# Performance work log

Hardware: AMD Instinct MI355X
Metric: run time of the kernel (lower is better)

## Reference

```python
import jax, jax.numpy as jnp
import numpy as np

B, H, W, C = 4, 128, 128, 180
HEADS, WS = 6, 16
HID = 720            # int(dim * mlp_ratio)
CONV_SCALE = 0.01
N = WS * WS          # tokens per window
CM = C // 2          # CAB mid channels (is_light_sr -> compress_ratio=2)
CS = C // 30         # channel-attention squeeze channels


def conv2d(x, w, b=None, padding=0, dilation=1, groups=1):
    out = jax.lax.conv_general_dilated(
        x, w, (1, 1), [(padding, padding), (padding, padding)],
        rhs_dilation=(dilation, dilation),
        dimension_numbers=('NCHW', 'OIHW', 'NCHW'),
        feature_group_count=groups)
    if b is not None:
        out = out + b[None, :, None, None]
    return out


def layernorm(x, g, b, eps=1e-5):
    mu = jnp.mean(x, -1, keepdims=True)
    var = jnp.var(x, -1, keepdims=True)
    return (x - mu) * jax.lax.rsqrt(var + eps) * g + b


def make_rpi(ws):
    coords = np.stack(np.meshgrid(np.arange(ws), np.arange(ws), indexing='ij'))
    cf = coords.reshape(2, -1)
    rel = (cf[:, :, None] - cf[:, None, :]).transpose(1, 2, 0).astype(np.int64)
    rel[:, :, 0] += ws - 1
    rel[:, :, 1] += ws - 1
    rel[:, :, 0] *= 2 * ws - 1
    return rel.sum(-1)  # [n, n]


def _forward(rpi_sa, x, norm1_g, norm1_b, rpb_table, qkv_w, qkv_b, proj_w, proj_b,
             cab_w0, cab_b0, cab_w1, cab_b1, cab_w2, cab_b2, cab_w3, cab_b3,
             ca_w1, ca_b1, ca_w2, ca_b2, norm2_g, norm2_b,
             fc1_w, fc1_b, dw_w, dw_b, pw_w, pw_b, sa_w, fc2_w, fc2_b):
    b = x.shape[0]
    shortcut = x
    xn = layernorm(x, norm1_g, norm1_b)
    x_img = xn.reshape(b, H, W, C)

    # --- window partition (shift_size=0 -> no roll, no mask) ---
    xw = x_img.reshape(b, H // WS, WS, W // WS, WS, C)
    xw = xw.transpose(0, 1, 3, 2, 4, 5).reshape(-1, N, C)  # [b*nW, n, C]

    # --- window attention with relative position bias ---
    hd = C // HEADS
    qkv = (xw @ qkv_w.T + qkv_b).reshape(-1, N, 3, HEADS, hd)
    qkv = qkv.transpose(2, 0, 3, 1, 4)  # [3, b*nW, heads, n, hd]
    q, k, v = qkv[0], qkv[1], qkv[2]
    attn = jnp.einsum('whnd,whmd->whnm', q * (hd ** -0.5), k)
    bias = rpb_table[rpi_sa.reshape(-1)].reshape(N, N, HEADS).transpose(2, 0, 1)
    attn = jax.nn.softmax(attn + bias[None], axis=-1)
    out = jnp.einsum('whnm,whmd->whnd', attn, v)
    out = out.transpose(0, 2, 1, 3).reshape(-1, N, C)
    out = out @ proj_w.T + proj_b

    # --- window reverse ---
    attn_x = out.reshape(b, H // WS, W // WS, WS, WS, C)
    attn_x = attn_x.transpose(0, 1, 3, 2, 4, 5).reshape(b, H * W, C)

    # --- CAB conv branch on norm1 output (light-SR variant) ---
    x2d = x_img.transpose(0, 3, 1, 2)  # NCHW
    y = conv2d(x2d, cab_w0, cab_b0)                                  # 1x1 C->C/2
    y = conv2d(y, cab_w1, cab_b1, padding=1, groups=CM)              # dw 3x3
    y = jax.nn.gelu(y, approximate=False)
    y = conv2d(y, cab_w2, cab_b2)                                    # 1x1 C/2->C
    y = conv2d(y, cab_w3, cab_b3, padding=2, dilation=2, groups=C)   # dw 3x3 dil2
    a = jnp.mean(y, (2, 3), keepdims=True)                           # GAP
    a = jax.nn.relu(conv2d(a, ca_w1, ca_b1))
    a = jax.nn.sigmoid(conv2d(a, ca_w2, ca_b2))
    conv_x = (y * a).transpose(0, 2, 3, 1).reshape(b, H * W, C)

    x = shortcut + attn_x + conv_x * CONV_SCALE

    # --- DSConvAttnFFN ---
    xn2 = layernorm(x, norm2_g, norm2_b)
    hdn = jax.nn.gelu(xn2 @ fc1_w.T + fc1_b, approximate=False)
    h2d = hdn.reshape(b, H, W, HID).transpose(0, 3, 1, 2)
    h2d = jax.nn.relu(conv2d(h2d, dw_w, dw_b, padding=1, groups=HID))
    h2d = jax.nn.relu(conv2d(h2d, pw_w, pw_b))
    mp = jnp.max(h2d, 1, keepdims=True)
    ap = jnp.mean(h2d, 1, keepdims=True)
    sa = jax.nn.sigmoid(conv2d(jnp.concatenate([mp, ap], 1), sa_w, padding=3))
    h2d = h2d * sa
    hdn = h2d.transpose(0, 2, 3, 1).reshape(b, H * W, HID)
    return x + (hdn @ fc2_w.T + fc2_b)


def setup_inputs():
    key = jax.random.key(0)
    ks = iter(jax.random.split(key, 48))
    def w(*shape):
        return jax.random.normal(next(ks), shape, jnp.float32) * 0.02
    return dict(
        x=jax.random.normal(next(ks), (B, H * W, C), jnp.float32),
        x_size_h=H, x_size_w=W,
        rpi_sa=jnp.asarray(make_rpi(WS)),
        norm1_g=jnp.ones((C,), jnp.float32), norm1_b=jnp.zeros((C,), jnp.float32),
        rpb_table=w((2 * WS - 1) ** 2, HEADS),
        qkv_w=w(3 * C, C), qkv_b=jnp.zeros((3 * C,), jnp.float32),
        proj_w=w(C, C), proj_b=jnp.zeros((C,), jnp.float32),
        cab_w0=w(CM, C, 1, 1), cab_b0=jnp.zeros((CM,), jnp.float32),
        cab_w1=w(CM, 1, 3, 3), cab_b1=jnp.zeros((CM,), jnp.float32),
        cab_w2=w(C, CM, 1, 1), cab_b2=jnp.zeros((C,), jnp.float32),
        cab_w3=w(C, 1, 3, 3), cab_b3=jnp.zeros((C,), jnp.float32),
        ca_w1=w(CS, C, 1, 1), ca_b1=jnp.zeros((CS,), jnp.float32),
        ca_w2=w(C, CS, 1, 1), ca_b2=jnp.zeros((C,), jnp.float32),
        norm2_g=jnp.ones((C,), jnp.float32), norm2_b=jnp.zeros((C,), jnp.float32),
        fc1_w=w(HID, C), fc1_b=jnp.zeros((HID,), jnp.float32),
        dw_w=w(HID, 1, 3, 3), dw_b=jnp.zeros((HID,), jnp.float32),
        pw_w=w(HID, HID, 1, 1), pw_b=jnp.zeros((HID,), jnp.float32),
        sa_w=w(1, 2, 7, 7),
        fc2_w=w(C, HID), fc2_b=jnp.zeros((C,), jnp.float32),
    )


def reference(x, x_size_h, x_size_w, rpi_sa, norm1_g, norm1_b, rpb_table,
              qkv_w, qkv_b, proj_w, proj_b,
              cab_w0, cab_b0, cab_w1, cab_b1, cab_w2, cab_b2, cab_w3, cab_b3,
              ca_w1, ca_b1, ca_w2, ca_b2, norm2_g, norm2_b,
              fc1_w, fc1_b, dw_w, dw_b, pw_w, pw_b, sa_w, fc2_w, fc2_b):
    del x_size_h, x_size_w  # fixed to H, W
    return _forward(rpi_sa, x, norm1_g, norm1_b, rpb_table, qkv_w, qkv_b,
                    proj_w, proj_b, cab_w0, cab_b0, cab_w1, cab_b1, cab_w2,
                    cab_b2, cab_w3, cab_b3, ca_w1, ca_b1, ca_w2, ca_b2,
                    norm2_g, norm2_b, fc1_w, fc1_b, dw_w, dw_b, pw_w, pw_b,
                    sa_w, fc2_w, fc2_b)
```

## Files before the change

### kernel.cpp

```cpp
#include <hip/hip_runtime.h>
#include <math.h>

#define HH 128
#define WW 128
#define CC 180
#define BB 4
#define IMG (HH*WW)
#define NTOK (BB*IMG)
#define HALFTOK (2*IMG)
#define NHEADS 6
#define HD 30
#define WSZ 16
#define NTOKW (WSZ*WSZ)
#define HID 720
#define QKVSTR 672

typedef __attribute__((ext_vector_type(8))) short short8v;
typedef __attribute__((ext_vector_type(4))) short short4v;
typedef __attribute__((ext_vector_type(4))) float f32x4;
typedef unsigned short ushortw;

__device__ __forceinline__ float warp_sum(float v) {
    #pragma unroll
    for (int o = 32; o > 0; o >>= 1) v += __shfl_xor(v, o);
    return v;
}
__device__ __forceinline__ float warp_max(float v) {
    #pragma unroll
    for (int o = 32; o > 0; o >>= 1) v = fmaxf(v, __shfl_xor(v, o));
    return v;
}
__device__ __forceinline__ float gelu_exact(float v) {
    return 0.5f * v * (1.f + erff(v * 0.70710678118654752f));
}
__device__ __forceinline__ ushortw f2bf(float f) {
    union { float f; unsigned int u; } c; c.f = f;
    unsigned int r = (c.u + 0x7FFFu + ((c.u >> 16) & 1u)) >> 16;
    return (ushortw)r;
}
__device__ __forceinline__ float bf2f(ushortw u) {
    union { unsigned int u; float f; } c; c.u = ((unsigned int)u) << 16; return c.f;
}

__global__ __launch_bounds__(256) void prep_kernel(
    const float* __restrict__ qkv_w, const float* __restrict__ proj_w,
    const float* __restrict__ cab_w0, const float* __restrict__ cab_b0,
    const float* __restrict__ cab_w2,
    const float* __restrict__ fc1_w, const float* __restrict__ pw_w,
    const float* __restrict__ fc2_w,
    const float* __restrict__ cab_w1, const float* __restrict__ cab_b1,
    const float* __restrict__ cab_w3, const float* __restrict__ cab_b3,
    const float* __restrict__ dw_w, const float* __restrict__ dw_b,
    const float* __restrict__ qkv_b, const int* __restrict__ rpi,
    const float* __restrict__ rpb,
    ushortw* __restrict__ wqkvc, ushortw* __restrict__ wproj,
    ushortw* __restrict__ wcab2,
    ushortw* __restrict__ wfc1, ushortw* __restrict__ wpw, ushortw* __restrict__ wfc2,
    float* __restrict__ dwt1, float* __restrict__ db1,
    float* __restrict__ dwt2, float* __restrict__ db2,
    float* __restrict__ dwt3, float* __restrict__ db3,
    float* __restrict__ qb672, float* __restrict__ biasN)
{
    int idx = blockIdx.x * 256 + threadIdx.x;
    if (idx < 129024) {
        int r = idx / 192, k = idx - r * 192;
        float v = 0.f;
        if (r < 576) {
            int sub = r / 192, rem = r - sub * 192;
            int hh = rem >> 5, dd = rem & 31;
            if (dd < 30 && k < 180) v = qkv_w[(sub * 180 + hh * 30 + dd) * 180 + k];
        } else if (r < 666) {
            if (k < 180) v = cab_w0[(r - 576) * 180 + k];
        }
        wqkvc[idx] = f2bf(v);
    } else if (idx < 178176) {
        int l = idx - 129024; int r = l / 192, k = l - r * 192;
        wproj[l] = f2bf((r < 180 && k < 180) ? proj_w[r * 180 + k] : 0.f);
    } else if (idx < 210944) {
        int l = idx - 178176; int r = l / 128, k = l - r * 128;
        wcab2[l] = f2bf((r < 180 && k < 90) ? cab_w2[r * 90 + k] : 0.f);
    } else if (idx < 358400) {
        int l = idx - 210944; int r = l / 192, k = l - r * 192;
        wfc1[l] = f2bf((r < 720 && k < 180) ? fc1_w[r * 180 + k] : 0.f);
    } else if (idx < 948224) {
        int l = idx - 358400; int r = l / 768, k = l - r * 768;
        wpw[l] = f2bf((r < 720 && k < 720) ? pw_w[r * 720 + k] : 0.f);
    } else if (idx < 1144832) {
        int l = idx - 948224; int r = l / 768, k = l - r * 768;
        wfc2[l] = f2bf((r < 180 && k < 720) ? fc2_w[r * 720 + k] : 0.f);
    } else if (idx < 1145984) {
        int l = idx - 1144832; int c = l / 9, k = l - c * 9;
        dwt1[k * 128 + c] = (c < 90) ? cab_w1[c * 9 + k] : 0.f;
        if (k == 0) db1[c] = (c < 90) ? cab_b1[c] : 0.f;
    } else if (idx < 1147712) {
        int l = idx - 1145984; int c = l / 9, k = l - c * 9;
        dwt2[k * 192 + c] = (c < 180) ? cab_w3[c * 9 + k] : 0.f;
        if (k == 0) db2[c] = (c < 180) ? cab_b3[c] : 0.f;
    } else if (idx < 1154624) {
        int l = idx - 1147712; int c = l / 9, k = l - c * 9;
        dwt3[k * 768 + c] = (c < 720) ? dw_w[c * 9 + k] : 0.f;
        if (k == 0) db3[c] = (c < 720) ? dw_b[c] : 0.f;
    } else if (idx < 1155296) {
        int l = idx - 1154624;
        float v = 0.f;
        if (l < 576) {
            int sub = l / 192, rem = l - sub * 192;
            int hh = rem >> 5, dd = rem & 31;
            if (dd < 30) v = qkv_b[sub * 180 + hh * 30 + dd];
        } else if (l < 666) {
            v = cab_b0[l - 576];
        }
        qb672[l] = v;
    } else if (idx < 1220832) {
        int l = idx - 1155296;
        int r = rpi[l];
        #pragma unroll
        for (int h = 0; h < NHEADS; h++)
            biasN[((size_t)h << 16) + l] = rpb[r * NHEADS + h];
    }
}

__global__ __launch_bounds__(256) void ln_kernel(
    const float* __restrict__ x, const float* __restrict__ g,
    const float* __restrict__ b, ushortw* __restrict__ out)
{
    int wid = threadIdx.x >> 6, lane = threadIdx.x & 63;
    int t = blockIdx.x * 4 + wid;
    size_t off = (size_t)t * CC;
    size_t off2 = (size_t)t * 192;
    bool has2 = lane < (CC - 128);
    float v0 = x[off + lane];
    float v1 = x[off + lane + 64];
    float v2 = has2 ? x[off + lane + 128] : 0.f;
    float s = warp_sum(v0 + v1 + v2);
    float mu = s * (1.f / CC);
    float d0 = v0 - mu, d1 = v1 - mu, d2 = has2 ? v2 - mu : 0.f;
    float var = warp_sum(d0*d0 + d1*d1 + d2*d2) * (1.f / CC);
    float rs = rsqrtf(var + 1e-5f);
    out[off2 + lane]      = f2bf(d0 * rs * g[lane]      + b[lane]);
    out[off2 + lane + 64] = f2bf(d1 * rs * g[lane + 64] + b[lane + 64]);
    out[off2 + lane + 128] = has2 ? f2bf(d2 * rs * g[lane + 128] + b[lane + 128]) : (ushortw)0;
}

__global__ __launch_bounds__(256) void mgemm_kernel(
    const ushortw* __restrict__ A, const ushortw* __restrict__ Wt,
    const float* __restrict__ bias, void* __restrict__ Cout,
    int M, int N, int Kp, int ldc, int outbf, int zfill, int act, int residbf, int nN,
    const float* __restrict__ rowscale, const void* __restrict__ residv)
{
    __shared__ ushortw sA[2][128 * 32];
    __shared__ ushortw sB[2][128 * 32];
    int tid = threadIdx.x, lane = tid & 63, wid = tid >> 6;
    int total = (int)gridDim.x;
    int orig = blockIdx.x;
    int q = total >> 3, r = total & 7;
    int xcd = orig & 7, slot = orig >> 3;
    int wgid = (xcd < r ? xcd * (q + 1) : r * (q + 1) + (xcd - r) * q) + slot;
    int mp = wgid / nN, np = wgid - mp * nN;
    int m0 = mp << 7, n0 = np << 7;
    int wm = (wid >> 1) << 6, wn = (wid & 1) << 6;
    int lrow = lane & 15, kgrp = lane >> 4;

    f32x4 acc[4][4];
    #pragma unroll
    for (int i = 0; i < 4; i++)
        #pragma unroll
        for (int j = 0; j < 4; j++)
            #pragma unroll
            for (int rr = 0; rr < 4; rr++) acc[i][j][rr] = 0.f;

    int nk = Kp >> 5;
    #pragma unroll
    for (int qq = 0; qq < 2; qq++) {
        int seg = (wid << 1) + qq;
        int row = (seg << 4) + (lane >> 2);
        int cg = (lane & 3) ^ (row & 3) ^ ((row >> 2) & 3);
        const ushortw* ga = A + (size_t)(m0 + row) * Kp + (cg << 3);
        __builtin_amdgcn_global_load_lds(
            (const __attribute__((address_space(1))) void*)ga,
            (__attribute__((address_space(3))) void*)&sA[0][seg << 9], 16, 0, 0);
        const ushortw* gb = Wt + (size_t)(n0 + row) * Kp + (cg << 3);
        __builtin_amdgcn_global_load_lds(
            (const __attribute__((address_space(1))) void*)gb,
            (__attribute__((address_space(3))) void*)&sB[0][seg << 9], 16, 0, 0);
    }
    __syncthreads();

    int cur = 0;
    for (int t = 0; t < nk; t++) {
        if (t + 1 < nk) {
            int kk2 = (t + 1) << 5;
            #pragma unroll
            for (int qq = 0; qq < 2; qq++) {
                int seg = (wid << 1) + qq;
                int row = (seg << 4) + (lane >> 2);
                int cg = (lane & 3) ^ (row & 3) ^ ((row >> 2) & 3);
                const ushortw* ga = A + (size_t)(m0 + row) * Kp + kk2 + (cg << 3);
                __builtin_amdgcn_global_load_lds(
                    (const __attribute__((address_space(1))) void*)ga,
                    (__attribute__((address_space(3))) void*)&sA[cur ^ 1][seg << 9], 16, 0, 0);
                const ushortw* gb = Wt + (size_t)(n0 + row) * Kp + kk2 + (cg << 3);
                __builtin_amdgcn_global_load_lds(
                    (const __attribute__((address_space(1))) void*)gb,
                    (__attribute__((address_space(3))) void*)&sB[cur ^ 1][seg << 9], 16, 0, 0);
            }
        }
        short8v a[4], b[4];
        #pragma unroll
        for (int i = 0; i < 4; i++) {
            int rr = wm + (i << 4) + lrow;
            int slot2 = kgrp ^ (rr & 3) ^ ((rr >> 2) & 3);
            a[i] = *reinterpret_cast<const short8v*>(&sA[cur][(rr << 5) + (slot2 << 3)]);
        }
        #pragma unroll
        for (int j = 0; j < 4; j++) {
            int rr = wn + (j << 4) + lrow;
            int slot2 = kgrp ^ (rr & 3) ^ ((rr >> 2) & 3);
            b[j] = *reinterpret_cast<const short8v*>(&sB[cur][(rr << 5) + (slot2 << 3)]);
        }
        #pragma unroll
        for (int i = 0; i < 4; i++)
            #pragma unroll
            for (int j = 0; j < 4; j++)
                acc[i][j] = __builtin_amdgcn_mfma_f32_16x16x32_bf16(a[i], b[j], acc[i][j], 0, 0, 0);
        __syncthreads();
        cur ^= 1;
    }
    #pragma unroll
    for (int i = 0; i < 4; i++) {
        int rowb = m0 + wm + (i << 4) + (kgrp << 2);
        #pragma unroll
        for (int j = 0; j < 4; j++) {
            int col = n0 + wn + (j << 4) + lrow;
            if (col < N) {
                float bi = bias[col];
                #pragma unroll
                for (int rr = 0; rr < 4; rr++) {
                    int row = rowb + rr;
                    float v = acc[i][j][rr];
                    if (rowscale) v *= rowscale[row];
                    v += bi;
                    if (act == 1) v = gelu_exact(v);
                    else if (act == 2) v = fmaxf(v, 0.f);
                    if (residv) {
                        v += residbf ? bf2f(((const ushortw*)residv)[(size_t)row * N + col])
                                     : ((const float*)residv)[(size_t)row * N + col];
                    }
                    if (outbf) ((ushortw*)Cout)[(size_t)row * ldc + col] = f2bf(v);
                    else       ((float*)Cout)[(size_t)row * ldc + col] = v;
                }
            } else if (zfill && col < ldc) {
                #pragma unroll
                for (int rr = 0; rr < 4; rr++) {
                    int row = rowb + rr;
                    if (outbf) ((ushortw*)Cout)[(size_t)row * ldc + col] = 0;
                    else       ((float*)Cout)[(size_t)row * ldc + col] = 0.f;
                }
            }
        }
    }
}

__global__ __launch_bounds__(256, 3) void attn_mfma_kernel(
    const ushortw* __restrict__ qkvP, const float* __restrict__ biasN,
    ushortw* __restrict__ out)
{
    __shared__ ushortw Vc[32 * 33 * 8];
    __shared__ ushortw Kc[256 * 32];
    __shared__ ushortw Pl[4][2048];
    const float SCALE = 0.18257418583505536f;
    int blk = blockIdx.x;
    int img = blk / 384;
    int rem = blk - img * 384;
    int win = rem / NHEADS;
    int h = rem - win * NHEADS;
    int base = img * IMG + (win >> 3) * WSZ * WW + (win & 7) * WSZ;
    int tid = threadIdx.x;
    int lane = tid & 63, w = tid >> 6;
    int a15 = lane & 15, kg = lane >> 4;

    {
        int j = tid;
        int g = base + (j >> 4) * WW + (j & 15);
        const ushortw* vp = qkvP + (size_t)g * QKVSTR + 384 + h * 32;
        short8v c0 = *reinterpret_cast<const short8v*>(vp);
        short8v c1 = *reinterpret_cast<const short8v*>(vp + 8);
        short8v c2 = *reinterpret_cast<const short8v*>(vp + 16);
        short8v c3 = *reinterpret_cast<const short8v*>(vp + 24);
        int bo = (j >> 3) * 264 + (j & 7);
        #pragma unroll
        for (int e = 0; e < 8; e++)  Vc[bo + (e) * 8]      = (ushortw)c0[e];
        #pragma unroll
        for (int e = 0; e < 8; e++)  Vc[bo + (8 + e) * 8]  = (ushortw)c1[e];
        #pragma unroll
        for (int e = 0; e < 8; e++)  Vc[bo + (16 + e) * 8] = (ushortw)c2[e];
        #pragma unroll
        for (int e = 0; e < 8; e++)  Vc[bo + (24 + e) * 8] = (ushortw)c3[e];
        const ushortw* kp = qkvP + (size_t)g * QKVSTR + 192 + h * 32;
        short8v k0 = *reinterpret_cast<const short8v*>(kp);
        short8v k1 = *reinterpret_cast<const short8v*>(kp + 8);
        short8v k2 = *reinterpret_cast<const short8v*>(kp + 16);
        short8v k3 = *reinterpret_cast<const short8v*>(kp + 24);
        short8v* krow = reinterpret_cast<short8v*>(&Kc[j * 32]);
        int jsw = j & 3;
        krow[0 ^ jsw] = k0; krow[1 ^ jsw] = k1; krow[2 ^ jsw] = k2; krow[3 ^ jsw] = k3;
    }
    __syncthreads();

    ushortw* Pw = &Pl[w][0];
    int xsw = (a15 & 7) << 2;
    f32x4 zf = {0.f, 0.f, 0.f, 0.f};
    #pragma unroll 1
    for (int si = 0; si < 4; si++) {
        int strip = (w << 2) + si;
        short8v qf = *reinterpret_cast<const short8v*>(
            qkvP + (size_t)(base + strip * WW + a15) * QKVSTR + h * 32 + (kg << 3));
        float psum = 0.f;
        f32x4 o0 = zf, o1 = zf;
        const float* brow = biasN + ((size_t)h << 16) + (size_t)((strip << 4) + a15) * 256;
        #pragma unroll 1
        for (int half = 0; half < 2; half++) {
            f32x4 s[8];
            __builtin_amdgcn_s_setprio(1);
            #pragma unroll
            for (int j8 = 0; j8 < 8; j8++) {
                int jt = (half << 3) + j8;
                int row = (jt << 4) + a15;
                short8v ka = reinterpret_cast<const short8v*>(&Kc[row * 32])[kg ^ (row & 3)];
                s[j8] = __builtin_amdgcn_mfma_f32_16x16x32_bf16(ka, qf, zf, 0, 0, 0);
            }
            __builtin_amdgcn_s_setprio(0);
            #pragma unroll
            for (int j8 = 0; j8 < 8; j8++) {
                int jt = (half << 3) + j8;
                float4 b4 = *reinterpret_cast<const float4*>(brow + (jt << 4) + (kg << 2));
                float p0 = __expf(fmaf(s[j8][0], SCALE, b4.x));
                float p1 = __expf(fmaf(s[j8][1], SCALE, b4.y));
                float p2 = __expf(fmaf(s[j8][2], SCALE, b4.z));
                float p3 = __expf(fmaf(s[j8][3], SCALE, b4.w));
                psum += (p0 + p1) + (p2 + p3);
                unsigned int u0, u1;
                asm("v_cvt_pk_bf16_f32 %0, %1, %2" : "=v"(u0) : "v"(p0), "v"(p1));
                asm("v_cvt_pk_bf16_f32 %0, %1, %2" : "=v"(u1) : "v"(p2), "v"(p3));
                int dw0 = ((j8 << 3) + (kg << 1)) ^ xsw;
                unsigned long long pk64 = (unsigned long long)u0 | ((unsigned long long)u1 << 32);
                *reinterpret_cast<unsigned long long*>(&Pw[(a15 << 7) + (dw0 << 1)]) = pk64;
            }
            __builtin_amdgcn_sched_barrier(0);
            __builtin_amdgcn_s_setprio(1);
            #pragma unroll
            for (int ks4 = 0; ks4 < 4; ks4++) {
                int dwr = ((ks4 << 4) + (kg << 2)) ^ xsw;
                short8v pa = *reinterpret_cast<const short8v*>(&Pw[(a15 << 7) + (dwr << 1)]);
                int kc = (((half << 2) + ks4) << 2) + kg;
                short8v v0 = *reinterpret_cast<const short8v*>(&Vc[(kc * 33 + a15) * 8]);
                short8v v1 = *reinterpret_cast<const short8v*>(&Vc[(kc * 33 + 16 + a15) * 8]);
                o0 = __builtin_amdgcn_mfma_f32_16x16x32_bf16(pa, v0, o0, 0, 0, 0);
                o1 = __builtin_amdgcn_mfma_f32_16x16x32_bf16(pa, v1, o1, 0, 0, 0);
            }
            __builtin_amdgcn_s_setprio(0);
            __builtin_amdgcn_sched_barrier(0);
        }
        psum += __shfl_xor(psum, 16);
        psum += __shfl_xor(psum, 32);
        #pragma unroll
        for (int r = 0; r < 4; r++) {
            float pt = __shfl(psum, (kg << 2) + r);
            float inv = 1.f / pt;
            int g = base + strip * WW + (kg << 2) + r;
            ushortw* orow = out + (size_t)g * 192 + h * HD;
            orow[a15] = f2bf(o0[r] * inv);
            if (a15 < 14) orow[16 + a15] = f2bf(o1[r] * inv);
        }
    }
    if (h == 0) {
        for (int idx2 = tid; idx2 < NTOKW * 12; idx2 += 256) {
            int j = idx2 / 12, d = idx2 - (idx2 / 12) * 12;
            int gj = base + (j >> 4) * WW + (j & 15);
            out[(size_t)gj * 192 + 180 + d] = 0;
        }
    }
}

template<int CIN_S, int COP, int OSTR, int DIL, int ACT, int OUTBF>
__global__ __launch_bounds__(256) void dwconv4_kernel(
    const ushortw* __restrict__ in, const float* __restrict__ wt,
    const float* __restrict__ bias, void* __restrict__ out)
{
    constexpr int NC4 = COP >> 2;
    constexpr int NX = 4 + 2 * DIL;
    int idx = blockIdx.x * 256 + threadIdx.x;
    int c4 = idx % NC4;
    int quad = idx / NC4;
    int c = c4 << 2;
    int pix0 = quad << 2;
    int p = pix0 & (IMG - 1);
    int imgbase = pix0 - p;
    int px0 = p & (WW - 1), py = p >> 7;

    float4 w9[9];
    #pragma unroll
    for (int t = 0; t < 9; t++)
        w9[t] = *reinterpret_cast<const float4*>(wt + t * COP + c);
    float4 bi4 = *reinterpret_cast<const float4*>(bias + c);
    float acc[4][4];
    #pragma unroll
    for (int i = 0; i < 4; i++) {
        acc[i][0] = bi4.x; acc[i][1] = bi4.y; acc[i][2] = bi4.z; acc[i][3] = bi4.w;
    }
    #pragma unroll
    for (int ky = 0; ky < 3; ky++) {
        int iy = py + (ky - 1) * DIL;
        if (iy < 0 || iy >= HH) continue;
        const ushortw* rowp = in + (size_t)(imgbase + (iy << 7)) * CIN_S + c;
        #pragma unroll
        for (int xx = 0; xx < NX; xx++) {
            int ix = px0 + xx - DIL;
            if (ix < 0 || ix >= WW) continue;
            short4v v = *reinterpret_cast<const short4v*>(rowp + (size_t)ix * CIN_S);
            float f0 = bf2f((ushortw)v[0]);
            float f1 = bf2f((ushortw)v[1]);
            float f2 = bf2f((ushortw)v[2]);
            float f3 = bf2f((ushortw)v[3]);
            #pragma unroll
            for (int kx = 0; kx < 3; kx++) {
                int i = xx - DIL * kx;
                if (i < 0 || i > 3) continue;
                float4 wv = w9[ky * 3 + kx];
                acc[i][0] = fmaf(f0, wv.x, acc[i][0]);
                acc[i][1] = fmaf(f1, wv.y, acc[i][1]);
                acc[i][2] = fmaf(f2, wv.z, acc[i][2]);
                acc[i][3] = fmaf(f3, wv.w, acc[i][3]);
            }
        }
    }
    if (COP != OSTR && c >= OSTR) return;
    #pragma unroll
    for (int i = 0; i < 4; i++) {
        #pragma unroll
        for (int e = 0; e < 4; e++) {
            float v = acc[i][e];
            if (ACT == 1) v = gelu_exact(v);
            else if (ACT == 2) v = fmaxf(v, 0.f);
            acc[i][e] = v;
        }
        if (OUTBF) {
            short4v o;
            o[0] = (short)f2bf(acc[i][0]); o[1] = (short)f2bf(acc[i][1]);
            o[2] = (short)f2bf(acc[i][2]); o[3] = (short)f2bf(acc[i][3]);
            *reinterpret_cast<short4v*>((ushortw*)out + (size_t)(pix0 + i) * OSTR + c) = o;
        } else {
            float4 o = make_float4(acc[i][0], acc[i][1], acc[i][2], acc[i][3]);
            *reinterpret_cast<float4*>((float*)out + (size_t)(pix0 + i) * OSTR + c) = o;
        }
    }
}

__global__ void gap_kernel(const ushortw* __restrict__ y, float* __restrict__ part)
{
    int blk = blockIdx.x;
    int b = blk >> 7, chunk = blk & 127;
    int c = threadIdx.x;
    if (c >= CC) return;
    size_t basep = ((size_t)b * IMG + (size_t)chunk * 128) * CC;
    float s = 0.f;
    for (int p = 0; p < 128; p++) s += bf2f(y[basep + (size_t)p * CC + c]);
    part[((size_t)b * 128 + chunk) * CC + c] = s;
}

__global__ void ca_kernel(const float* __restrict__ part,
                          const float* __restrict__ w1, const float* __restrict__ b1,
                          const float* __restrict__ w2, const float* __restrict__ b2,
                          float* __restrict__ ca)
{
    __shared__ float gap[BB * CC];
    __shared__ float s1[BB * 6];
    int tid = threadIdx.x;
    for (int idx = tid; idx < BB * CC; idx += 256) {
        int b = idx / CC, c = idx % CC;
        float s = 0.f;
        for (int ch = 0; ch < 128; ch++) s += part[((size_t)b * 128 + ch) * CC + c];
        gap[idx] = s * (1.f / IMG);
    }
    __syncthreads();
    if (tid < BB * 6) {
        int b = tid / 6, cs = tid % 6;
        float s = 0.f;
        for (int c = 0; c < CC; c++) s += w1[cs * CC + c] * gap[b * CC + c];
        s1[tid] = fmaxf(s + b1[cs], 0.f);
    }
    __syncthreads();
    for (int idx = tid; idx < BB * CC; idx += 256) {
        int b = idx / CC, c = idx % CC;
        float s = b2[c];
        #pragma unroll
        for (int cs = 0; cs < 6; cs++) s += w2[c * 6 + cs] * s1[b * 6 + cs];
        ca[idx] = 1.f / (1.f + __expf(-s));
    }
}

__global__ __launch_bounds__(256) void resid_ln_kernel(
    ushortw* __restrict__ x1, const ushortw* __restrict__ y4, const float* __restrict__ ca,
    const float* __restrict__ g, const float* __restrict__ bb,
    ushortw* __restrict__ xn2)
{
    int wid = threadIdx.x >> 6, lane = threadIdx.x & 63;
    int t = blockIdx.x * 4 + wid;
    int b = t >> 14;
    size_t off = (size_t)t * CC;
    size_t off2 = (size_t)t * 192;
    bool has2 = lane < (CC - 128);
    float v0 = bf2f(x1[off+lane])    + 0.01f * bf2f(y4[off+lane])    * ca[b*CC + lane];
    float v1 = bf2f(x1[off+lane+64]) + 0.01f * bf2f(y4[off+lane+64]) * ca[b*CC + lane+64];
    float v2 = 0.f;
    if (has2) v2 = bf2f(x1[off+lane+128]) + 0.01f * bf2f(y4[off+lane+128]) * ca[b*CC + lane+128];
    x1[off+lane] = f2bf(v0); x1[off+lane+64] = f2bf(v1);
    if (has2) x1[off+lane+128] = f2bf(v2);
    float s = warp_sum(v0 + v1 + v2);
    float mu = s * (1.f / CC);
    float d0 = v0-mu, d1 = v1-mu, d2 = has2 ? v2-mu : 0.f;
    float var = warp_sum(d0*d0 + d1*d1 + d2*d2) * (1.f / CC);
    float rs = rsqrtf(var + 1e-5f);
    xn2[off2+lane]      = f2bf(d0 * rs * g[lane]      + bb[lane]);
    xn2[off2+lane+64]   = f2bf(d1 * rs * g[lane+64]   + bb[lane+64]);
    xn2[off2+lane+128]  = has2 ? f2bf(d2 * rs * g[lane+128] + bb[lane+128]) : (ushortw)0;
}

__global__ __launch_bounds__(256) void mpap_kernel(
    const ushortw* __restrict__ h, float* __restrict__ mp, float* __restrict__ ap)
{
    int wid = threadIdx.x >> 6, lane = threadIdx.x & 63;
    int p = blockIdx.x * 4 + wid;
    const ushortw* row = h + (size_t)p * 768;
    float mx = -1e30f, s = 0.f;
    for (int j = lane; j < HID; j += 64) { float v = bf2f(row[j]); mx = fmaxf(mx, v); s += v; }
    mx = warp_max(mx); s = warp_sum(s);
    if (lane == 0) { mp[p] = mx; ap[p] = s * (1.f / HID); }
}

__global__ void saconv_kernel(const float* __restrict__ mp, const float* __restrict__ ap,
                              const float* __restrict__ w, float* __restrict__ sa)
{
    int p = blockIdx.x * blockDim.x + threadIdx.x;
    int lp = p & (IMG - 1);
    int base = p - lp;
    int px = lp & (WW - 1), py = lp >> 7;
    float acc = 0.f;
    for (int ky = 0; ky < 7; ky++) {
        int iy = py + ky - 3;
        if (iy < 0 || iy >= HH) continue;
        for (int kx = 0; kx < 7; kx++) {
            int ix = px + kx - 3;
            if (ix < 0 || ix >= WW) continue;
            int pid = base + iy * WW + ix;
            acc += mp[pid] * w[ky * 7 + kx] + ap[pid] * w[49 + ky * 7 + kx];
        }
    }
    sa[p] = 1.f / (1.f + __expf(-acc));
}

extern "C" void kernel_launch(void* const* d_in, const int* in_sizes, int n_in,
                              void* d_out, int out_size, void* d_ws, size_t ws_size,
                              hipStream_t stream)
{
    const float* x      = (const float*)d_in[0];
    const int*   rpi    = (const int*)d_in[3];
    const float* n1g    = (const float*)d_in[4];
    const float* n1b    = (const float*)d_in[5];
    const float* rpb    = (const float*)d_in[6];
    const float* qkv_w  = (const float*)d_in[7];
    const float* qkv_b  = (const float*)d_in[8];
    const float* proj_w = (const float*)d_in[9];
    const float* proj_b = (const float*)d_in[10];
    const float* cab_w0 = (const float*)d_in[11];
    const float* cab_b0 = (const float*)d_in[12];
    const float* cab_w1 = (const float*)d_in[13];
    const float* cab_b1 = (const float*)d_in[14];
    const float* cab_w2 = (const float*)d_in[15];
    const float* cab_b2 = (const float*)d_in[16];
    const float* cab_w3 = (const float*)d_in[17];
    const float* cab_b3 = (const float*)d_in[18];
    const float* ca_w1  = (const float*)d_in[19];
    const float* ca_b1  = (const float*)d_in[20];
    const float* ca_w2  = (const float*)d_in[21];
    const float* ca_b2  = (const float*)d_in[22];
    const float* n2g    = (const float*)d_in[23];
    const float* n2b    = (const float*)d_in[24];
    const float* fc1_w  = (const float*)d_in[25];
    const float* fc1_b  = (const float*)d_in[26];
    const float* dw_w   = (const float*)d_in[27];
    const float* dw_b   = (const float*)d_in[28];
    const float* pw_w   = (const float*)d_in[29];
    const float* pw_b   = (const float*)d_in[30];
    const float* sa_w   = (const float*)d_in[31];
    const float* fc2_w  = (const float*)d_in[32];
    const float* fc2_b  = (const float*)d_in[33];
    float* outp = (float*)d_out;
    (void)in_sizes; (void)n_in; (void)out_size; (void)ws_size;

    char* ws = (char*)d_ws;
    const size_t S0 = (size_t)NTOK * 192 * 2;
    const size_t S1 = (size_t)NTOK * QKVSTR * 2 + 256;
    const size_t S2 = (size_t)NTOK * 192 * 2;
    const size_t S3 = (size_t)NTOK * 180 * 2;
    const size_t S4 = (size_t)NTOK * 128 * 2;
    const size_t S5 = (size_t)NTOK * 180 * 4;
    char* pA0 = ws;
    char* pA1 = pA0 + S0;
    char* pA2 = pA1 + S1;
    char* pA3 = pA2 + S2;
    char* pA4 = pA3 + S3;
    char* pA5 = pA4 + S4;
    char* tail = pA5 + S5;

    ushortw* xnb    = (ushortw*)pA0;
    ushortw* xn2b   = (ushortw*)pA0;
    ushortw* qkvP   = (ushortw*)pA1;
    ushortw* h1     = (ushortw*)pA1;
    ushortw* h3     = (ushortw*)pA1;
    ushortw* attnbb = (ushortw*)pA2;
    ushortw* y3b    = (ushortw*)pA2;
    ushortw* x1b    = (ushortw*)pA3;
    ushortw* y2b    = (ushortw*)pA4;
    ushortw* h2     = (ushortw*)pA4;
    ushortw* y4     = (ushortw*)pA5;

    ushortw* wqkvc = (ushortw*)tail;
    ushortw* wproj = wqkvc + 672 * 192;
    ushortw* wcab2 = wproj + 256 * 192;
    ushortw* wfc1  = wcab2 + 256 * 128;
    ushortw* wpw   = wfc1  + 768 * 192;
    ushortw* wfc2  = wpw   + 768 * 768;
    char* tail2 = (char*)(wfc2 + 256 * 768);
    float* dwt1 = (float*)tail2;                 float* db1 = dwt1 + 9*128;
    float* dwt2 = db1 + 128;                     float* db2 = dwt2 + 9*192;
    float* dwt3 = db2 + 192;                     float* db3 = dwt3 + 9*768;
    float* qb672 = db3 + 768;
    char* tail3 = (char*)(qb672 + 672);
    float* biasN = (float*)tail3;
    float* part  = (float*)(tail3 + 1572864);
    float* cabuf = (float*)(tail3 + 1572864 + 393216);
    float* mp    = (float*)(tail3 + 1572864 + 393216 + 4096);
    float* ap    = (float*)(tail3 + 1572864 + 393216 + 4096 + (size_t)HALFTOK * 4);
    float* sab   = (float*)(tail3 + 1572864 + 393216 + 4096 + 2*(size_t)HALFTOK * 4);

    auto gemm = [&](const ushortw* A, const ushortw* Wt, const float* bi, void* Cp,
                    int M, int N, int Kp, int ldc, int outbf, int zfill, int act, int residbf,
                    const float* rs, const void* resid) {
        int nM = M >> 7, nN = (N + 127) >> 7;
        mgemm_kernel<<<dim3(nM * nN), dim3(256), 0, stream>>>(
            A, Wt, bi, Cp, M, N, Kp, ldc, outbf, zfill, act, residbf, nN, rs, resid);
    };

    prep_kernel<<<dim3((1220832 + 255) / 256), dim3(256), 0, stream>>>(
        qkv_w, proj_w, cab_w0, cab_b0, cab_w2, fc1_w, pw_w, fc2_w,
        cab_w1, cab_b1, cab_w3, cab_b3, dw_w, dw_b, qkv_b, rpi, rpb,
        wqkvc, wproj, wcab2, wfc1, wpw, wfc2,
        dwt1, db1, dwt2, db2, dwt3, db3, qb672, biasN);

    ln_kernel<<<dim3(NTOK / 4), dim3(256), 0, stream>>>(x, n1g, n1b, xnb);
    gemm(xnb, wqkvc, qb672, qkvP, NTOK, 672, 192, QKVSTR, 1, 0, 0, 0, nullptr, nullptr);
    attn_mfma_kernel<<<dim3(BB * 64 * NHEADS), dim3(256), 0, stream>>>(qkvP, biasN, attnbb);
    dwconv4_kernel<672, 128, 128, 1, 1, 1><<<dim3(NTOK / 4 * 32 / 256), dim3(256), 0, stream>>>(
        qkvP + 576, dwt1, db1, y2b);
    gemm(attnbb, wproj, proj_b, x1b, NTOK, 180, 192, 180, 1, 0, 0, 0, nullptr, x);
    gemm(y2b, wcab2, cab_b2, y3b, NTOK, 180, 128, 192, 1, 1, 0, 0, nullptr, nullptr);
    dwconv4_kernel<192, 192, 180, 2, 0, 1><<<dim3(NTOK / 4 * 48 / 256), dim3(256), 0, stream>>>(
        y3b, dwt2, db2, y4);
    gap_kernel<<<dim3(BB * 128), dim3(192), 0, stream>>>(y4, part);
    ca_kernel<<<dim3(1), dim3(256), 0, stream>>>(part, ca_w1, ca_b1, ca_w2, ca_b2, cabuf);
    resid_ln_kernel<<<dim3(NTOK / 4), dim3(256), 0, stream>>>(x1b, y4, cabuf, n2g, n2b, xn2b);
    for (int half = 0; half < 2; half++) {
        size_t toff = (size_t)half * HALFTOK;
        gemm(xn2b + toff * 192, wfc1, fc1_b, h1, HALFTOK, 720, 192, 720, 1, 0, 1, 0, nullptr, nullptr);
        dwconv4_kernel<720, 768, 768, 1, 2, 1><<<dim3(HALFTOK / 4 * 192 / 256), dim3(256), 0, stream>>>(
            h1, dwt3, db3, h2);
        gemm(h2, wpw, pw_b, h3, HALFTOK, 720, 768, 768, 1, 1, 2, 0, nullptr, nullptr);
        mpap_kernel<<<dim3(HALFTOK / 4), dim3(256), 0, stream>>>(h3, mp, ap);
        saconv_kernel<<<dim3(HALFTOK / 256), dim3(256), 0, stream>>>(mp, ap, sa_w, sab);
        gemm(h3, wfc2, fc2_b, outp + toff * 180, HALFTOK, 180, 768, 180, 0, 0, 0, 1,
             sab, x1b + toff * 180);
    }
}
```

Before: 754.9 us.

## Change GEMM LDS layout to segmented k-major and feed bf16 residual

```diff
diff --git a/kernel.cpp b/kernel.cpp
--- a/kernel.cpp
+++ b/kernel.cpp
@@ -122,7 +122,7 @@
 
 __global__ __launch_bounds__(256) void ln_kernel(
     const float* __restrict__ x, const float* __restrict__ g,
-    const float* __restrict__ b, ushortw* __restrict__ out)
+    const float* __restrict__ b, ushortw* __restrict__ out, ushortw* __restrict__ xb)
 {
     int wid = threadIdx.x >> 6, lane = threadIdx.x & 63;
     int t = blockIdx.x * 4 + wid;
@@ -132,6 +132,9 @@
     float v0 = x[off + lane];
     float v1 = x[off + lane + 64];
     float v2 = has2 ? x[off + lane + 128] : 0.f;
+    xb[off + lane] = f2bf(v0);
+    xb[off + lane + 64] = f2bf(v1);
+    if (has2) xb[off + lane + 128] = f2bf(v2);
     float s = warp_sum(v0 + v1 + v2);
     float mu = s * (1.f / CC);
     float d0 = v0 - mu, d1 = v1 - mu, d2 = has2 ? v2 - mu : 0.f;
@@ -161,6 +164,9 @@
     int wm = (wid >> 1) << 6, wn = (wid & 1) << 6;
     int lrow = lane & 15, kgrp = lane >> 4;
 
+    int srow = lane & 15;
+    int sko  = (lane >> 4) << 3;
+
     f32x4 acc[4][4];
     #pragma unroll
     for (int i = 0; i < 4; i++)
@@ -173,13 +179,12 @@
     #pragma unroll
     for (int qq = 0; qq < 2; qq++) {
         int seg = (wid << 1) + qq;
-        int row = (seg << 4) + (lane >> 2);
-        int cg = (lane & 3) ^ (row & 3) ^ ((row >> 2) & 3);
-        const ushortw* ga = A + (size_t)(m0 + row) * Kp + (cg << 3);
+        int row = (seg << 4) + srow;
+        const ushortw* ga = A + (size_t)(m0 + row) * Kp + sko;
         __builtin_amdgcn_global_load_lds(
             (const __attribute__((address_space(1))) void*)ga,
             (__attribute__((address_space(3))) void*)&sA[0][seg << 9], 16, 0, 0);
-        const ushortw* gb = Wt + (size_t)(n0 + row) * Kp + (cg << 3);
+        const ushortw* gb = Wt + (size_t)(n0 + row) * Kp + sko;
         __builtin_amdgcn_global_load_lds(
             (const __attribute__((address_space(1))) void*)gb,
             (__attribute__((address_space(3))) void*)&sB[0][seg << 9], 16, 0, 0);
@@ -193,13 +198,12 @@
             #pragma unroll
             for (int qq = 0; qq < 2; qq++) {
                 int seg = (wid << 1) + qq;
-                int row = (seg << 4) + (lane >> 2);
-                int cg = (lane & 3) ^ (row & 3) ^ ((row >> 2) & 3);
-                const ushortw* ga = A + (size_t)(m0 + row) * Kp + kk2 + (cg << 3);
+                int row = (seg << 4) + srow;
+                const ushortw* ga = A + (size_t)(m0 + row) * Kp + kk2 + sko;
                 __builtin_amdgcn_global_load_lds(
                     (const __attribute__((address_space(1))) void*)ga,
                     (__attribute__((address_space(3))) void*)&sA[cur ^ 1][seg << 9], 16, 0, 0);
-                const ushortw* gb = Wt + (size_t)(n0 + row) * Kp + kk2 + (cg << 3);
+                const ushortw* gb = Wt + (size_t)(n0 + row) * Kp + kk2 + sko;
                 __builtin_amdgcn_global_load_lds(
                     (const __attribute__((address_space(1))) void*)gb,
                     (__attribute__((address_space(3))) void*)&sB[cur ^ 1][seg << 9], 16, 0, 0);
@@ -209,14 +213,14 @@
         #pragma unroll
         for (int i = 0; i < 4; i++) {
             int rr = wm + (i << 4) + lrow;
-            int slot2 = kgrp ^ (rr & 3) ^ ((rr >> 2) & 3);
-            a[i] = *reinterpret_cast<const short8v*>(&sA[cur][(rr << 5) + (slot2 << 3)]);
+            a[i] = *reinterpret_cast<const short8v*>(
+                &sA[cur][((rr >> 4) << 9) + (kgrp << 7) + ((rr & 15) << 3)]);
         }
         #pragma unroll
         for (int j = 0; j < 4; j++) {
             int rr = wn + (j << 4) + lrow;
-            int slot2 = kgrp ^ (rr & 3) ^ ((rr >> 2) & 3);
-            b[j] = *reinterpret_cast<const short8v*>(&sB[cur][(rr << 5) + (slot2 << 3)]);
+            b[j] = *reinterpret_cast<const short8v*>(
+                &sB[cur][((rr >> 4) << 9) + (kgrp << 7) + ((rr & 15) << 3)]);
         }
         #pragma unroll
         for (int i = 0; i < 4; i++)
@@ -623,6 +627,7 @@
     ushortw* x1b    = (ushortw*)pA3;
     ushortw* y2b    = (ushortw*)pA4;
     ushortw* h2     = (ushortw*)pA4;
+    ushortw* xb     = (ushortw*)pA5;
     ushortw* y4     = (ushortw*)pA5;
 
     ushortw* wqkvc = (ushortw*)tail;
@@ -658,12 +663,12 @@
         wqkvc, wproj, wcab2, wfc1, wpw, wfc2,
         dwt1, db1, dwt2, db2, dwt3, db3, qb672, biasN);
 
-    ln_kernel<<<dim3(NTOK / 4), dim3(256), 0, stream>>>(x, n1g, n1b, xnb);
+    ln_kernel<<<dim3(NTOK / 4), dim3(256), 0, stream>>>(x, n1g, n1b, xnb, xb);
     gemm(xnb, wqkvc, qb672, qkvP, NTOK, 672, 192, QKVSTR, 1, 0, 0, 0, nullptr, nullptr);
     attn_mfma_kernel<<<dim3(BB * 64 * NHEADS), dim3(256), 0, stream>>>(qkvP, biasN, attnbb);
     dwconv4_kernel<672, 128, 128, 1, 1, 1><<<dim3(NTOK / 4 * 32 / 256), dim3(256), 0, stream>>>(
         qkvP + 576, dwt1, db1, y2b);
-    gemm(attnbb, wproj, proj_b, x1b, NTOK, 180, 192, 180, 1, 0, 0, 0, nullptr, x);
+    gemm(attnbb, wproj, proj_b, x1b, NTOK, 180, 192, 180, 1, 0, 0, 1, nullptr, xb);
     gemm(y2b, wcab2, cab_b2, y3b, NTOK, 180, 128, 192, 1, 1, 0, 0, nullptr, nullptr);
     dwconv4_kernel<192, 192, 180, 2, 0, 1><<<dim3(NTOK / 4 * 48 / 256), dim3(256), 0, stream>>>(
         y3b, dwt2, db2, y4);
```

After: 834.3 us. 1.11x slower.
